# Optimization experiments

Measured on AMD Instinct MI355X. Metric: run time of the kernel, lower is better.

Reference implementation:

```python
import jax, jax.numpy as jnp
import numpy as np

N = 6144      # num_sample / nodes per graph
E = 196608    # edges per graph (avg degree 32)
F = 256       # input feature dim (same for all 4 graphs)
H = 256       # hidden_channels (== F so all SAGEConv layers are HxH)
D = 512       # fusion dim (hardcoded in module)
G = 4         # number of graphs
ATT = 128     # attention bottleneck (hardcoded)
WS = 0.05     # weight init scale


def setup_inputs() -> dict:
    key = jax.random.key(0)
    k = jax.random.split(key, 16)
    return {
        "xs": jax.random.normal(k[0], (G, N, F), jnp.float32),
        "edge_index": jax.random.randint(k[1], (G, 2, E), 0, N),
        "x_content": jax.random.normal(k[2], (N, F), jnp.float32),
        # SAGEConv params: per graph, 3 layers, lin_l (with bias) on aggregated
        # neighbors, lin_r (no bias) on root. F == H so all layers stack.
        "sage_Wl": jax.random.normal(k[3], (G, 3, H, H), jnp.float32) * WS,
        "sage_bl": jnp.zeros((G, 3, H), jnp.float32),
        "sage_Wr": jax.random.normal(k[4], (G, 3, H, H), jnp.float32) * WS,
        # lin1..lin4 : F -> 512
        "lin_W": jax.random.normal(k[5], (G, D, F), jnp.float32) * WS,
        "lin_b": jnp.zeros((G, D), jnp.float32),
        # ResidualFusion attention MLP 512 -> 128 -> 1, softmax over graph axis
        "att_W1": jax.random.normal(k[6], (ATT, D), jnp.float32) * WS,
        "att_b1": jnp.zeros((ATT,), jnp.float32),
        "att_W2": jax.random.normal(k[7], (1, ATT), jnp.float32) * WS,
        "att_b2": jnp.zeros((1,), jnp.float32),
        "res_W": jax.random.normal(k[8], (D, D), jnp.float32) * WS,
        "res_b": jnp.zeros((D,), jnp.float32),
        "fusion_weight": jnp.array([0.7, 0.3], jnp.float32),
        # SelfExpression coefficients, init 1e-8 * ones as in the module
        "C_content": jnp.full((N, N), 1e-8, jnp.float32),
        "C_structure": jnp.full((N, N), 1e-8, jnp.float32),
    }


def _gnn(x, ei, Wl, bl, Wr):
    # One GraphSAGE stack: 3 SAGEConv(mean) layers, relu after each,
    # dropout is identity in eval mode.
    src, dst = ei[0], ei[1]
    deg = jax.ops.segment_sum(jnp.ones((E,), x.dtype), dst, num_segments=N)
    deg = jnp.maximum(deg, 1.0)[:, None]
    for i in range(3):
        m = jax.ops.segment_sum(x[src], dst, num_segments=N) / deg  # mean aggr
        x = jax.nn.relu(m @ Wl[i].T + bl[i] + x @ Wr[i].T)
    return x


def reference(xs, edge_index, x_content, sage_Wl, sage_bl, sage_Wr,
              lin_W, lin_b, att_W1, att_b1, att_W2, att_b2,
              res_W, res_b, fusion_weight, C_content, C_structure):
    # Four GraphSAGE stacks, vmapped over the graph axis.
    xg = jax.vmap(_gnn)(xs, edge_index, sage_Wl, sage_bl, sage_Wr)  # [G,N,F]
    # lin1..lin4 -> [G,N,D]
    feats = jnp.einsum('gnf,gdf->gnd', xg, lin_W) + lin_b[:, None, :]
    # ResidualFusion: attention over stacked features, softmax over graph axis
    h = jax.nn.relu(jnp.einsum('gnd,kd->gnk', feats, att_W1) + att_b1)
    logits = jnp.einsum('gnk,ok->gno', h, att_W2) + att_b2  # [G,N,1]
    w = jax.nn.softmax(logits, axis=0)
    weighted = jnp.sum(w * feats, axis=0)            # [N,D]
    residual = feats[0] @ res_W.T + res_b            # [N,D]
    structure_features = jax.nn.relu(weighted + residual)
    # Coefficient fusion with softmax-normalized scalar weights
    fw = jax.nn.softmax(fusion_weight)
    fusion_expression = fw[0] * C_content + fw[1] * C_structure  # [N,N]
    return (fusion_expression, x_content, structure_features, C_content, C_structure)
```

## Files before the change

### kernel.cpp

```cpp
#include <hip/hip_runtime.h>
#include <hip/hip_bf16.h>

constexpr int N_ = 6144;
constexpr int E_ = 196608;
constexpr int F_ = 256;
constexpr int D_ = 512;
constexpr int G_ = 4;
constexpr int A_ = 128;

typedef short bf16x8 __attribute__((ext_vector_type(8)));
typedef float f32x4 __attribute__((ext_vector_type(4)));
typedef float f4 __attribute__((ext_vector_type(4)));
typedef int i4 __attribute__((ext_vector_type(4)));
typedef __hip_bfloat16 hb;

__device__ inline float b2f(unsigned short u) {
    union { unsigned u32; float f; } x; x.u32 = ((unsigned)u) << 16; return x.f;
}
__device__ inline unsigned short f2bu(float f) {
    hb b = __float2bfloat16(f);
    return *reinterpret_cast<unsigned short*>(&b);
}

#define GLD_LDS16(gp, lp) \
    __builtin_amdgcn_global_load_lds((const __attribute__((address_space(1))) void*)(gp), \
                                     (__attribute__((address_space(3))) void*)(lp), 16, 0, 0)

struct SP {
    const f4* Cc; const f4* Cs; const float* fw;
    f4* o0; f4* o3; f4* o4;
    long ib; long ie; int nsb;
};

__device__ void stream_slice(const SP sp, int sb)
{
    float fa = sp.fw[0], fb = sp.fw[1];
    float mx = fmaxf(fa, fb);
    float ea = expf(fa - mx), eb = expf(fb - mx);
    float w0 = ea / (ea + eb), w1 = eb / (ea + eb);
    const long S = (long)sp.nsb * blockDim.x;
    long i = sp.ib + (long)sb * blockDim.x + threadIdx.x;
    for (; i + 3 * S < sp.ie; i += 4 * S) {
        f4 a0 = __builtin_nontemporal_load(sp.Cc + i);
        f4 b0 = __builtin_nontemporal_load(sp.Cs + i);
        f4 a1 = __builtin_nontemporal_load(sp.Cc + i + S);
        f4 b1 = __builtin_nontemporal_load(sp.Cs + i + S);
        f4 a2 = __builtin_nontemporal_load(sp.Cc + i + 2 * S);
        f4 b2 = __builtin_nontemporal_load(sp.Cs + i + 2 * S);
        f4 a3 = __builtin_nontemporal_load(sp.Cc + i + 3 * S);
        f4 b3 = __builtin_nontemporal_load(sp.Cs + i + 3 * S);
        __builtin_nontemporal_store(a0, sp.o3 + i);
        __builtin_nontemporal_store(b0, sp.o4 + i);
        __builtin_nontemporal_store(w0 * a0 + w1 * b0, sp.o0 + i);
        __builtin_nontemporal_store(a1, sp.o3 + i + S);
        __builtin_nontemporal_store(b1, sp.o4 + i + S);
        __builtin_nontemporal_store(w0 * a1 + w1 * b1, sp.o0 + i + S);
        __builtin_nontemporal_store(a2, sp.o3 + i + 2 * S);
        __builtin_nontemporal_store(b2, sp.o4 + i + 2 * S);
        __builtin_nontemporal_store(w0 * a2 + w1 * b2, sp.o0 + i + 2 * S);
        __builtin_nontemporal_store(a3, sp.o3 + i + 3 * S);
        __builtin_nontemporal_store(b3, sp.o4 + i + 3 * S);
        __builtin_nontemporal_store(w0 * a3 + w1 * b3, sp.o0 + i + 3 * S);
    }
    for (; i < sp.ie; i += S) {
        f4 a = __builtin_nontemporal_load(sp.Cc + i);
        f4 b = __builtin_nontemporal_load(sp.Cs + i);
        __builtin_nontemporal_store(a, sp.o3 + i);
        __builtin_nontemporal_store(b, sp.o4 + i);
        __builtin_nontemporal_store(w0 * a + w1 * b, sp.o0 + i);
    }
}

__global__ void k_tail(SP sp) { stream_slice(sp, blockIdx.x); }

__global__ void k_prep(const float* __restrict__ xc, f4* __restrict__ o1,
                       const float* __restrict__ xs, ushort4* __restrict__ xsb,
                       const float* __restrict__ Wl, ushort4* __restrict__ Wlb,
                       const float* __restrict__ Wr, ushort4* __restrict__ Wrb,
                       const float* __restrict__ lin, ushort4* __restrict__ linb,
                       const float* __restrict__ aw, ushort4* __restrict__ awb,
                       const float* __restrict__ rw, ushort4* __restrict__ rwb,
                       i4* __restrict__ cursz, int PB, SP sp)
{
    if ((int)blockIdx.x < sp.nsb) { stream_slice(sp, blockIdx.x); return; }
    const int cb = blockIdx.x - sp.nsb;
    const long nz = (long)G_ * N_ / 4;
    const long n0 = (long)N_ * F_ / 4;
    const long n1 = (long)G_ * N_ * F_ / 4;
    const long n2 = (long)G_ * 3 * F_ * F_ / 4;
    const long n4 = (long)G_ * D_ * F_ / 4;
    const long n5 = (long)A_ * D_ / 4;
    const long n6 = (long)D_ * D_ / 4;
    const long T = nz + n0 + n1 + 2 * n2 + n4 + n5 + n6;
    long stride = (long)PB * blockDim.x;
    for (long u = (long)cb * blockDim.x + threadIdx.x; u < T; u += stride) {
        long v = u;
        if (v < nz) { cursz[v] = i4{0, 0, 0, 0}; continue; }
        v -= nz;
        if (v < n0) {
            f4 x = __builtin_nontemporal_load((const f4*)xc + v);
            __builtin_nontemporal_store(x, o1 + v);
            continue;
        }
        v -= n0;
        const float* s; ushort4* d;
        if (v < n1) { s = xs; d = xsb; }
        else {
            v -= n1;
            if (v < n2) { s = Wl; d = Wlb; }
            else {
                v -= n2;
                if (v < n2) { s = Wr; d = Wrb; }
                else {
                    v -= n2;
                    if (v < n4) { s = lin; d = linb; }
                    else {
                        v -= n4;
                        if (v < n5) { s = aw; d = awb; }
                        else { v -= n5; s = rw; d = rwb; }
                    }
                }
            }
        }
        f4 x = *((const f4*)s + v);
        ushort4 o;
        o.x = f2bu(x[0]); o.y = f2bu(x[1]); o.z = f2bu(x[2]); o.w = f2bu(x[3]);
        d[v] = o;
    }
}

__global__ void k_count(const int* __restrict__ ei, int* __restrict__ cnt, SP sp)
{
    if ((int)blockIdx.x < sp.nsb) { stream_slice(sp, blockIdx.x); return; }
    long i = (long)(blockIdx.x - sp.nsb) * blockDim.x + threadIdx.x;
    int g = (int)(i / E_);
    int e = (int)(i % E_);
    int dst = ei[(long)g * 2 * E_ + E_ + e];
    atomicAdd(&cnt[g * N_ + dst], 1);
}

__global__ void k_scan(int* __restrict__ cnt_cursor, int* __restrict__ row_ptr,
                       float* __restrict__ deg, SP sp)
{
    if ((int)blockIdx.x < sp.nsb) { stream_slice(sp, blockIdx.x); return; }
    int g = blockIdx.x - sp.nsb;
    __shared__ int swsum[16];
    __shared__ int s_off;
    const int lane = threadIdx.x & 63;
    const int wid = threadIdx.x >> 6;
    if (threadIdx.x == 0) s_off = 0;
    __syncthreads();
    for (int base = 0; base < N_; base += 1024) {
        int idx = g * N_ + base + threadIdx.x;
        int v = cnt_cursor[idx];
        int incl = v;
        #pragma unroll
        for (int d = 1; d < 64; d <<= 1) {
            int t = __shfl_up(incl, d);
            if (lane >= d) incl += t;
        }
        if (lane == 63) swsum[wid] = incl;
        __syncthreads();
        if (wid == 0 && lane < 16) {
            int sv = swsum[lane];
            #pragma unroll
            for (int d = 1; d < 16; d <<= 1) {
                int t = __shfl_up(sv, d);
                if (lane >= d) sv += t;
            }
            swsum[lane] = sv;
        }
        __syncthreads();
        int bse = s_off;
        int woff = wid ? swsum[wid - 1] : 0;
        int rp = bse + woff + incl - v;
        row_ptr[g * (N_ + 1) + base + threadIdx.x] = rp;
        cnt_cursor[idx] = rp;
        deg[idx] = (float)(v > 1 ? v : 1);
        __syncthreads();
        if (threadIdx.x == 0) s_off = bse + swsum[15];
        __syncthreads();
    }
    if (threadIdx.x == 0) row_ptr[g * (N_ + 1) + N_] = s_off;
}

__global__ void k_fill(const int* __restrict__ ei, int* __restrict__ cursor,
                       int* __restrict__ csr_src, SP sp)
{
    if ((int)blockIdx.x < sp.nsb) { stream_slice(sp, blockIdx.x); return; }
    long i = (long)(blockIdx.x - sp.nsb) * blockDim.x + threadIdx.x;
    int g = (int)(i / E_);
    int e = (int)(i % E_);
    int src = ei[(long)g * 2 * E_ + e];
    int dst = ei[(long)g * 2 * E_ + E_ + e];
    int pos = atomicAdd(&cursor[g * N_ + dst], 1);
    csr_src[(long)g * E_ + pos] = src;
}

__global__ __launch_bounds__(256) void k_aggregate(
    const hb* __restrict__ x, const int* __restrict__ csr_src,
    const int* __restrict__ row_ptr, const float* __restrict__ deg,
    hb* __restrict__ m, SP sp)
{
    if ((int)blockIdx.x < sp.nsb) { stream_slice(sp, blockIdx.x); return; }
    int b = blockIdx.x - sp.nsb;
    int g = (b & 7) >> 1;
    int idx = ((b >> 3) << 1) | (b & 1);
    int node = idx * 4 + (threadIdx.x >> 6);
    int lane = threadIdx.x & 63;
    int qq = lane >> 4;
    int l16 = (lane & 15) * 16;
    const hb* xg = x + (long)g * N_ * F_;
    const int* rp = row_ptr + g * (N_ + 1);
    const int* cs = csr_src + (long)g * E_;
    int s = __builtin_amdgcn_readfirstlane(rp[node]);
    int e = __builtin_amdgcn_readfirstlane(rp[node + 1]);
    float a[16] = {};
    #pragma unroll 4
    for (int j = s; j < e; j += 4) {
        if (j + qq < e) {
            int src = cs[j + qq];
            const bf16x8* p = (const bf16x8*)(xg + (long)src * F_ + l16);
            bf16x8 v0 = p[0], v1 = p[1];
            #pragma unroll
            for (int q = 0; q < 8; ++q) a[q]     += b2f((unsigned short)v0[q]);
            #pragma unroll
            for (int q = 0; q < 8; ++q) a[q + 8] += b2f((unsigned short)v1[q]);
        }
    }
    #pragma unroll
    for (int q = 0; q < 16; ++q) {
        a[q] += __shfl_xor(a[q], 16);
        a[q] += __shfl_xor(a[q], 32);
    }
    if (qq == 0) {
        float inv = 1.0f / deg[g * N_ + node];
        bf16x8 lo, hi;
        #pragma unroll
        for (int q = 0; q < 8; ++q) { lo[q] = (short)f2bu(a[q] * inv); hi[q] = (short)f2bu(a[q + 8] * inv); }
        *(bf16x8*)(m + ((long)g * N_ + node) * F_ + l16) = lo;
        *(bf16x8*)(m + ((long)g * N_ + node) * F_ + l16 + 8) = hi;
    }
}

template <bool DUAL, bool RELU, bool LOGITS, bool FUSEOUT, bool PIN>
__global__ __launch_bounds__(256) void k_mfma_nt(
    const hb* __restrict__ A1, const hb* __restrict__ B1,
    const hb* __restrict__ A2, const hb* __restrict__ B2,
    const float* __restrict__ bias, hb* __restrict__ C,
    int ncols, int nrows, int ng, int Nc, int K,
    long a_batch, long b_batch, long bias_batch, long c_batch,
    const float* __restrict__ W2, const float* __restrict__ b2,
    float* __restrict__ logits,
    const float* __restrict__ lgAll, const hb* __restrict__ fAll,
    float* __restrict__ o2,
    SP sp)
{
    if ((int)blockIdx.x < sp.nsb) { stream_slice(sp, blockIdx.x); return; }
    int b = blockIdx.x - sp.nsb;
    int g, col, row;
    if (PIN) {
        g = (b & 7) >> 1;
        int idx = ((b >> 3) << 1) | (b & 1);
        col = idx % ncols; row = idx / ncols;
    } else {
        col = b % ncols;
        int r2 = b / ncols;
        row = r2 % nrows; g = r2 / nrows;
    }
    const int row0 = row * 128;
    const int col0 = col * 128;

    const hb* A1p = A1 + (long)g * a_batch;
    const hb* B1p = B1 + (long)g * b_batch;
    const hb* A2p = nullptr;
    const hb* B2p = nullptr;
    if (DUAL) { A2p = A2 + (long)g * a_batch; B2p = B2 + (long)g * b_batch; }
    const float* biasp = bias + (long)g * bias_batch;
    hb* Cp = C + (long)g * c_batch;

    __shared__ hb As[128 * 64];
    __shared__ hb Bs[128 * 64];
    __shared__ float sLog[2][128];
    __shared__ float sW[128][4];

    const int tid = threadIdx.x;
    const int lane = tid & 63;
    const int wid = tid >> 6;
    const int wr = wid >> 1;
    const int wc = wid & 1;

    if (FUSEOUT) {
        if (tid < 128) {
            int rr = row0 + tid;
            float l0 = lgAll[rr], l1 = lgAll[N_ + rr], l2 = lgAll[2 * N_ + rr], l3 = lgAll[3 * N_ + rr];
            float mx = fmaxf(fmaxf(l0, l1), fmaxf(l2, l3));
            float e0 = expf(l0 - mx), e1 = expf(l1 - mx), e2 = expf(l2 - mx), e3 = expf(l3 - mx);
            float inv = 1.f / (e0 + e1 + e2 + e3);
            sW[tid][0] = e0 * inv; sW[tid][1] = e1 * inv;
            sW[tid][2] = e2 * inv; sW[tid][3] = e3 * inv;
        }
    }

    const int srow = tid >> 3;
    const int sk8  = (tid & 7) * 8;

    f32x4 acc[4][4] = {};

    const int fr  = lane & 15;
    const int fkq = (lane >> 4) * 8;

    const int npass = DUAL ? 2 : 1;
    for (int pass = 0; pass < npass; ++pass) {
        const hb* A = (DUAL && pass) ? A2p : A1p;
        const hb* B = (DUAL && pass) ? B2p : B1p;
        for (int k0 = 0; k0 < K; k0 += 64) {
            __syncthreads();
            #pragma unroll
            for (int c = 0; c < 4; ++c) {
                int r = c * 32 + srow;
                GLD_LDS16(A + (long)(row0 + r) * K + k0 + sk8, As + r * 64 + sk8);
                GLD_LDS16(B + (long)(col0 + r) * K + k0 + sk8, Bs + r * 64 + sk8);
            }
            __syncthreads();

            bf16x8 af[4][2], bfr[4][2];
            #pragma unroll
            for (int m = 0; m < 4; ++m)
                #pragma unroll
                for (int kk = 0; kk < 2; ++kk)
                    af[m][kk] = *(const bf16x8*)(As + (wr * 64 + m * 16 + fr) * 64 + kk * 32 + fkq);
            #pragma unroll
            for (int n = 0; n < 4; ++n)
                #pragma unroll
                for (int kk = 0; kk < 2; ++kk)
                    bfr[n][kk] = *(const bf16x8*)(Bs + (wc * 64 + n * 16 + fr) * 64 + kk * 32 + fkq);

            #pragma unroll
            for (int m = 0; m < 4; ++m)
                #pragma unroll
                for (int n = 0; n < 4; ++n)
                    #pragma unroll
                    for (int kk = 0; kk < 2; ++kk)
                        acc[m][n] = __builtin_amdgcn_mfma_f32_16x16x32_bf16(
                            af[m][kk], bfr[n][kk], acc[m][n], 0, 0, 0);
        }
    }

    const int r4 = (lane >> 4) * 4;
    const int cc = lane & 15;

    if (LOGITS) {
        float w2v[4], bv[4];
        #pragma unroll
        for (int n = 0; n < 4; ++n) {
            int c2 = wc * 64 + n * 16 + cc;
            w2v[n] = W2[c2];
            bv[n]  = biasp[c2];
        }
        #pragma unroll
        for (int m = 0; m < 4; ++m) {
            #pragma unroll
            for (int j = 0; j < 4; ++j) {
                float p = 0.f;
                #pragma unroll
                for (int n = 0; n < 4; ++n) {
                    float h = fmaxf(acc[m][n][j] + bv[n], 0.f);
                    p += h * w2v[n];
                }
                p += __shfl_xor(p, 1); p += __shfl_xor(p, 2);
                p += __shfl_xor(p, 4); p += __shfl_xor(p, 8);
                if (cc == 0) sLog[wc][wr * 64 + m * 16 + r4 + j] = p;
            }
        }
        __syncthreads();
        if (tid < 128)
            logits[(long)g * N_ + row0 + tid] = sLog[0][tid] + sLog[1][tid] + b2[0];
    } else if (FUSEOUT) {
        const unsigned short* fu = (const unsigned short*)fAll;
        #pragma unroll
        for (int m = 0; m < 4; ++m) {
            #pragma unroll
            for (int n = 0; n < 4; ++n) {
                int c2 = col0 + wc * 64 + n * 16 + cc;
                float bv = biasp[c2];
                #pragma unroll
                for (int j = 0; j < 4; ++j) {
                    int rl = wr * 64 + m * 16 + r4 + j;
                    int rr = row0 + rl;
                    float s = acc[m][n][j] + bv;
                    #pragma unroll
                    for (int gg = 0; gg < 4; ++gg)
                        s += sW[rl][gg] * b2f(fu[((long)gg * N_ + rr) * D_ + c2]);
                    __builtin_nontemporal_store(fmaxf(s, 0.f), o2 + (long)rr * D_ + c2);
                }
            }
        }
    } else {
        #pragma unroll
        for (int m = 0; m < 4; ++m) {
            #pragma unroll
            for (int n = 0; n < 4; ++n) {
                int c2 = col0 + wc * 64 + n * 16 + cc;
                float bv = biasp[c2];
                #pragma unroll
                for (int j = 0; j < 4; ++j) {
                    int rr = row0 + wr * 64 + m * 16 + r4 + j;
                    float v = acc[m][n][j] + bv;
                    if (RELU) v = fmaxf(v, 0.f);
                    Cp[(long)rr * Nc + c2] = __float2bfloat16(v);
                }
            }
        }
    }
}

extern "C" void kernel_launch(void* const* d_in, const int* in_sizes, int n_in,
                              void* d_out, int out_size, void* d_ws, size_t ws_size,
                              hipStream_t stream)
{
    const float* xs        = (const float*)d_in[0];
    const int*   ei        = (const int*)  d_in[1];
    const float* x_content = (const float*)d_in[2];
    const float* sage_Wl   = (const float*)d_in[3];
    const float* sage_bl   = (const float*)d_in[4];
    const float* sage_Wr   = (const float*)d_in[5];
    const float* lin_W     = (const float*)d_in[6];
    const float* lin_b     = (const float*)d_in[7];
    const float* att_W1    = (const float*)d_in[8];
    const float* att_b1    = (const float*)d_in[9];
    const float* att_W2    = (const float*)d_in[10];
    const float* att_b2    = (const float*)d_in[11];
    const float* res_W     = (const float*)d_in[12];
    const float* res_b     = (const float*)d_in[13];
    const float* fusion_w  = (const float*)d_in[14];
    const float* Cc        = (const float*)d_in[15];
    const float* Cs        = (const float*)d_in[16];

    float* out0 = (float*)d_out;
    float* out1 = out0 + (size_t)N_ * N_;
    float* out2 = out1 + (size_t)N_ * F_;
    float* out3 = out2 + (size_t)N_ * D_;
    float* out4 = out3 + (size_t)N_ * N_;

    char* w = (char*)d_ws;
    auto alloc = [&](size_t bytes) {
        char* p = w;
        w += (bytes + 255) & ~(size_t)255;
        return p;
    };
    hb* xsb   = (hb*)alloc((size_t)G_ * N_ * F_ * 2);
    hb* xA    = (hb*)alloc((size_t)G_ * N_ * F_ * 2);
    hb* xB    = (hb*)alloc((size_t)G_ * N_ * F_ * 2);
    hb* mb    = (hb*)alloc((size_t)G_ * N_ * F_ * 2);
    hb* feats = (hb*)alloc((size_t)G_ * N_ * D_ * 2);
    hb* Wlb   = (hb*)alloc((size_t)G_ * 3 * F_ * F_ * 2);
    hb* Wrb   = (hb*)alloc((size_t)G_ * 3 * F_ * F_ * 2);
    hb* linWb = (hb*)alloc((size_t)G_ * D_ * F_ * 2);
    hb* attWb = (hb*)alloc((size_t)A_ * D_ * 2);
    hb* resWb = (hb*)alloc((size_t)D_ * D_ * 2);
    float* logit = (float*)alloc((size_t)G_ * N_ * 4);
    float* deg   = (float*)alloc((size_t)G_ * N_ * 4);
    int*   rowp  = (int*)  alloc((size_t)G_ * (N_ + 1) * 4);
    int*   curs  = (int*)  alloc((size_t)G_ * N_ * 4);
    int*   csrc  = (int*)  alloc((size_t)G_ * E_ * 4);

    const long U = (long)N_ * N_ / 4;
    const int cum[14] = {0, 85, 110, 130, 160, 255, 325, 420, 490, 585, 655, 745, 815, 950};
    long B[14];
    for (int i = 0; i < 14; ++i) B[i] = U * cum[i] / 1000;
    const int PREPB   = 512;
    const int SB_PREP = 512;
    const int SB_FLAT = 256;
    const int SB_GEMM = 256;
    const int TAILB   = 1024;
    auto mkSP = [&](int i, int nsb) {
        SP sp;
        sp.Cc = (const f4*)Cc; sp.Cs = (const f4*)Cs; sp.fw = fusion_w;
        sp.o0 = (f4*)out0; sp.o3 = (f4*)out3; sp.o4 = (f4*)out4;
        sp.ib = B[i]; sp.ie = (i == 13) ? U : B[i + 1]; sp.nsb = nsb;
        return sp;
    };
    SP tail = mkSP(13, TAILB);

    k_prep<<<SB_PREP + PREPB, 256, 0, stream>>>(
        x_content, (f4*)out1, xs, (ushort4*)xsb,
        sage_Wl, (ushort4*)Wlb, sage_Wr, (ushort4*)Wrb,
        lin_W, (ushort4*)linWb, att_W1, (ushort4*)attWb, res_W, (ushort4*)resWb,
        (i4*)curs, PREPB, mkSP(0, SB_PREP));

    k_count<<<SB_FLAT + G_ * E_ / 256, 256, 0, stream>>>(ei, curs, mkSP(1, SB_FLAT));
    k_scan<<<SB_FLAT + G_, 1024, 0, stream>>>(curs, rowp, deg, mkSP(2, SB_FLAT));
    k_fill<<<SB_FLAT + G_ * E_ / 256, 256, 0, stream>>>(ei, curs, csrc, mkSP(3, SB_FLAT));

    const hb* xin = xsb;
    hb* xout = xA;
    for (int layer = 0; layer < 3; ++layer) {
        k_aggregate<<<SB_FLAT + G_ * N_ / 4, 256, 0, stream>>>(
            xin, csrc, rowp, deg, mb, mkSP(4 + 2 * layer, SB_FLAT));
        k_mfma_nt<true, true, false, false, true>
            <<<SB_GEMM + (F_ / 128) * (N_ / 128) * G_, 256, 0, stream>>>(
            mb, Wlb + (size_t)layer * F_ * F_,
            xin, Wrb + (size_t)layer * F_ * F_,
            sage_bl + (size_t)layer * F_, xout,
            F_ / 128, N_ / 128, G_, F_, F_,
            (long)N_ * F_, (long)3 * F_ * F_, (long)3 * F_, (long)N_ * F_,
            nullptr, nullptr, nullptr, nullptr, nullptr, nullptr,
            mkSP(5 + 2 * layer, SB_GEMM));
        xin = xout;
        xout = (layer == 0) ? xB : xA;
    }
    const hb* xg = xA;

    k_mfma_nt<false, false, false, false, true>
        <<<SB_GEMM + (D_ / 128) * (N_ / 128) * G_, 256, 0, stream>>>(
        xg, linWb, nullptr, nullptr, lin_b, feats,
        D_ / 128, N_ / 128, G_, D_, F_,
        (long)N_ * F_, (long)D_ * F_, (long)D_, (long)N_ * D_,
        nullptr, nullptr, nullptr, nullptr, nullptr, nullptr,
        mkSP(10, SB_GEMM));

    k_mfma_nt<false, true, true, false, true>
        <<<SB_GEMM + (A_ / 128) * (N_ / 128) * G_, 256, 0, stream>>>(
        feats, attWb, nullptr, nullptr, att_b1, nullptr,
        A_ / 128, N_ / 128, G_, A_, D_,
        (long)N_ * D_, 0L, 0L, 0L,
        att_W2, att_b2, logit, nullptr, nullptr, nullptr,
        mkSP(11, SB_GEMM));

    k_mfma_nt<false, false, false, true, false>
        <<<SB_GEMM + (D_ / 128) * (N_ / 128) * 1, 256, 0, stream>>>(
        feats, resWb, nullptr, nullptr, res_b, nullptr,
        D_ / 128, N_ / 128, 1, D_, D_,
        0L, 0L, 0L, 0L,
        nullptr, nullptr, nullptr, logit, feats, out2,
        mkSP(12, SB_GEMM));

    k_tail<<<TAILB, 256, 0, stream>>>(tail);
}
```

Before: 422.9 us.

## Fold edge counting into prep, add 128x64 SAGE GEMM, rebalance stream slices

Merges the degree-count atomics into the prep kernel and zeroes the counters with a memset instead, removing one launch. Adds a dedicated SAGE layer GEMM with 128x64 tiles, which doubles the block count to improve occupancy on the small F=256 output. Unrolls the copy and convert loops by four. Re-tunes how the N×N streaming work is split across kernels and changes the prep block counts. This adds code size and more atomic contention within the single prep kernel.

```diff
diff --git a/kernel.cpp b/kernel.cpp
--- a/kernel.cpp
+++ b/kernel.cpp
@@ -11,7 +11,6 @@
 typedef short bf16x8 __attribute__((ext_vector_type(8)));
 typedef float f32x4 __attribute__((ext_vector_type(4)));
 typedef float f4 __attribute__((ext_vector_type(4)));
-typedef int i4 __attribute__((ext_vector_type(4)));
 typedef __hip_bfloat16 hb;
 
 __device__ inline float b2f(unsigned short u) {
@@ -20,6 +19,11 @@
 __device__ inline unsigned short f2bu(float f) {
     hb b = __float2bfloat16(f);
     return *reinterpret_cast<unsigned short*>(&b);
+}
+__device__ inline ushort4 cvt4(f4 x) {
+    ushort4 o;
+    o.x = f2bu(x[0]); o.y = f2bu(x[1]); o.z = f2bu(x[2]); o.w = f2bu(x[3]);
+    return o;
 }
 
 #define GLD_LDS16(gp, lp) \
@@ -80,33 +84,56 @@
                        const float* __restrict__ lin, ushort4* __restrict__ linb,
                        const float* __restrict__ aw, ushort4* __restrict__ awb,
                        const float* __restrict__ rw, ushort4* __restrict__ rwb,
-                       i4* __restrict__ cursz, int PB, SP sp)
+                       const int* __restrict__ ei, int* __restrict__ cnt,
+                       int PB, SP sp)
 {
     if ((int)blockIdx.x < sp.nsb) { stream_slice(sp, blockIdx.x); return; }
     const int cb = blockIdx.x - sp.nsb;
-    const long nz = (long)G_ * N_ / 4;
-    const long n0 = (long)N_ * F_ / 4;
-    const long n1 = (long)G_ * N_ * F_ / 4;
-    const long n2 = (long)G_ * 3 * F_ * F_ / 4;
-    const long n4 = (long)G_ * D_ * F_ / 4;
-    const long n5 = (long)A_ * D_ / 4;
-    const long n6 = (long)D_ * D_ / 4;
-    const long T = nz + n0 + n1 + 2 * n2 + n4 + n5 + n6;
-    long stride = (long)PB * blockDim.x;
-    for (long u = (long)cb * blockDim.x + threadIdx.x; u < T; u += stride) {
-        long v = u;
-        if (v < nz) { cursz[v] = i4{0, 0, 0, 0}; continue; }
-        v -= nz;
-        if (v < n0) {
-            f4 x = __builtin_nontemporal_load((const f4*)xc + v);
-            __builtin_nontemporal_store(x, o1 + v);
-            continue;
-        }
-        v -= n0;
-        const float* s; ushort4* d;
-        if (v < n1) { s = xs; d = xsb; }
-        else {
-            v -= n1;
+    const long S = (long)PB * 256;
+    const long t0 = (long)cb * 256 + threadIdx.x;
+
+    {
+        const long n = (long)N_ * F_ / 4;
+        const f4* src = (const f4*)xc;
+        long i = t0;
+        for (; i + 3 * S < n; i += 4 * S) {
+            f4 x0 = __builtin_nontemporal_load(src + i);
+            f4 x1 = __builtin_nontemporal_load(src + i + S);
+            f4 x2 = __builtin_nontemporal_load(src + i + 2 * S);
+            f4 x3 = __builtin_nontemporal_load(src + i + 3 * S);
+            __builtin_nontemporal_store(x0, o1 + i);
+            __builtin_nontemporal_store(x1, o1 + i + S);
+            __builtin_nontemporal_store(x2, o1 + i + 2 * S);
+            __builtin_nontemporal_store(x3, o1 + i + 3 * S);
+        }
+        for (; i < n; i += S)
+            __builtin_nontemporal_store(__builtin_nontemporal_load(src + i), o1 + i);
+    }
+    {
+        const long n = (long)G_ * N_ * F_ / 4;
+        const f4* src = (const f4*)xs;
+        long i = t0;
+        for (; i + 3 * S < n; i += 4 * S) {
+            f4 x0 = src[i];
+            f4 x1 = src[i + S];
+            f4 x2 = src[i + 2 * S];
+            f4 x3 = src[i + 3 * S];
+            xsb[i] = cvt4(x0);
+            xsb[i + S] = cvt4(x1);
+            xsb[i + 2 * S] = cvt4(x2);
+            xsb[i + 3 * S] = cvt4(x3);
+        }
+        for (; i < n; i += S) xsb[i] = cvt4(src[i]);
+    }
+    {
+        const long n2 = (long)G_ * 3 * F_ * F_ / 4;
+        const long n4 = (long)G_ * D_ * F_ / 4;
+        const long n5 = (long)A_ * D_ / 4;
+        const long n6 = (long)D_ * D_ / 4;
+        const long T = 2 * n2 + n4 + n5 + n6;
+        for (long u = t0; u < T; u += S) {
+            long v = u;
+            const float* s; ushort4* d;
             if (v < n2) { s = Wl; d = Wlb; }
             else {
                 v -= n2;
@@ -121,22 +148,17 @@
                     }
                 }
             }
-        }
-        f4 x = *((const f4*)s + v);
-        ushort4 o;
-        o.x = f2bu(x[0]); o.y = f2bu(x[1]); o.z = f2bu(x[2]); o.w = f2bu(x[3]);
-        d[v] = o;
-    }
-}
-
-__global__ void k_count(const int* __restrict__ ei, int* __restrict__ cnt, SP sp)
-{
-    if ((int)blockIdx.x < sp.nsb) { stream_slice(sp, blockIdx.x); return; }
-    long i = (long)(blockIdx.x - sp.nsb) * blockDim.x + threadIdx.x;
-    int g = (int)(i / E_);
-    int e = (int)(i % E_);
-    int dst = ei[(long)g * 2 * E_ + E_ + e];
-    atomicAdd(&cnt[g * N_ + dst], 1);
+            d[v] = cvt4(((const f4*)s)[v]);
+        }
+    }
+    {
+        for (long i = t0; i < (long)G_ * E_; i += S) {
+            int g = (int)(i / E_);
+            int e = (int)(i % E_);
+            int dst = ei[(long)g * 2 * E_ + E_ + e];
+            atomicAdd(&cnt[g * N_ + dst], 1);
+        }
+    }
 }
 
 __global__ void k_scan(int* __restrict__ cnt_cursor, int* __restrict__ row_ptr,
@@ -243,10 +265,101 @@
     }
 }
 
-template <bool DUAL, bool RELU, bool LOGITS, bool FUSEOUT, bool PIN>
+__global__ __launch_bounds__(256) void k_sage64(
+    const hb* __restrict__ A1, const hb* __restrict__ B1,
+    const hb* __restrict__ A2, const hb* __restrict__ B2,
+    const float* __restrict__ bias, hb* __restrict__ C, SP sp)
+{
+    if ((int)blockIdx.x < sp.nsb) { stream_slice(sp, blockIdx.x); return; }
+    int b = blockIdx.x - sp.nsb;
+    int g = (b & 7) >> 1;
+    int idx = ((b >> 3) << 1) | (b & 1);
+    int col = idx & 3, row = idx >> 2;
+    const int row0 = row * 128, col0 = col * 64;
+
+    const hb* A1p = A1 + (long)g * N_ * F_;
+    const hb* A2p = A2 + (long)g * N_ * F_;
+    const hb* B1p = B1 + (long)g * 3 * F_ * F_;
+    const hb* B2p = B2 + (long)g * 3 * F_ * F_;
+    const float* biasp = bias + (long)g * 3 * F_;
+    hb* Cp = C + (long)g * N_ * F_;
+
+    __shared__ hb As[128 * 64];
+    __shared__ hb Bs[64 * 64];
+
+    const int tid = threadIdx.x;
+    const int lane = tid & 63;
+    const int wid = tid >> 6;
+    const int wr = wid >> 1, wc = wid & 1;
+    const int srow = tid >> 3;
+    const int sk8 = (tid & 7) * 8;
+    const int fr = lane & 15;
+    const int fkq = (lane >> 4) * 8;
+
+    f32x4 acc[4][2] = {};
+
+    #pragma unroll
+    for (int pass = 0; pass < 2; ++pass) {
+        const hb* A = pass ? A2p : A1p;
+        const hb* B = pass ? B2p : B1p;
+        for (int k0 = 0; k0 < F_; k0 += 64) {
+            __syncthreads();
+            #pragma unroll
+            for (int c = 0; c < 4; ++c) {
+                int r = c * 32 + srow;
+                GLD_LDS16(A + (long)(row0 + r) * F_ + k0 + sk8, As + r * 64 + sk8);
+            }
+            #pragma unroll
+            for (int c = 0; c < 2; ++c) {
+                int r = c * 32 + srow;
+                GLD_LDS16(B + (long)(col0 + r) * F_ + k0 + sk8, Bs + r * 64 + sk8);
+            }
+            __syncthreads();
+
+            bf16x8 af[4][2], bq[2][2];
+            #pragma unroll
+            for (int m = 0; m < 4; ++m)
+                #pragma unroll
+                for (int kk = 0; kk < 2; ++kk)
+                    af[m][kk] = *(const bf16x8*)(As + (wr * 64 + m * 16 + fr) * 64 + kk * 32 + fkq);
+            #pragma unroll
+            for (int n = 0; n < 2; ++n)
+                #pragma unroll
+                for (int kk = 0; kk < 2; ++kk)
+                    bq[n][kk] = *(const bf16x8*)(Bs + (wc * 32 + n * 16 + fr) * 64 + kk * 32 + fkq);
+
+            #pragma unroll
+            for (int m = 0; m < 4; ++m)
+                #pragma unroll
+                for (int n = 0; n < 2; ++n)
+                    #pragma unroll
+                    for (int kk = 0; kk < 2; ++kk)
+                        acc[m][n] = __builtin_amdgcn_mfma_f32_16x16x32_bf16(
+                            af[m][kk], bq[n][kk], acc[m][n], 0, 0, 0);
+        }
+    }
+
+    const int r4 = (lane >> 4) * 4;
+    const int cc = lane & 15;
+    #pragma unroll
+    for (int m = 0; m < 4; ++m) {
+        #pragma unroll
+        for (int n = 0; n < 2; ++n) {
+            int c2 = col0 + wc * 32 + n * 16 + cc;
+            float bv = biasp[c2];
+            #pragma unroll
+            for (int j = 0; j < 4; ++j) {
+                int rr = row0 + wr * 64 + m * 16 + r4 + j;
+                float v = fmaxf(acc[m][n][j] + bv, 0.f);
+                Cp[(long)rr * F_ + c2] = __float2bfloat16(v);
+            }
+        }
+    }
+}
+
+template <bool RELU, bool LOGITS, bool FUSEOUT, bool PIN>
 __global__ __launch_bounds__(256) void k_mfma_nt(
     const hb* __restrict__ A1, const hb* __restrict__ B1,
-    const hb* __restrict__ A2, const hb* __restrict__ B2,
     const float* __restrict__ bias, hb* __restrict__ C,
     int ncols, int nrows, int ng, int Nc, int K,
     long a_batch, long b_batch, long bias_batch, long c_batch,
@@ -273,9 +386,6 @@
 
     const hb* A1p = A1 + (long)g * a_batch;
     const hb* B1p = B1 + (long)g * b_batch;
-    const hb* A2p = nullptr;
-    const hb* B2p = nullptr;
-    if (DUAL) { A2p = A2 + (long)g * a_batch; B2p = B2 + (long)g * b_batch; }
     const float* biasp = bias + (long)g * bias_batch;
     hb* Cp = C + (long)g * c_batch;
 
@@ -310,41 +420,36 @@
     const int fr  = lane & 15;
     const int fkq = (lane >> 4) * 8;
 
-    const int npass = DUAL ? 2 : 1;
-    for (int pass = 0; pass < npass; ++pass) {
-        const hb* A = (DUAL && pass) ? A2p : A1p;
-        const hb* B = (DUAL && pass) ? B2p : B1p;
-        for (int k0 = 0; k0 < K; k0 += 64) {
-            __syncthreads();
-            #pragma unroll
-            for (int c = 0; c < 4; ++c) {
-                int r = c * 32 + srow;
-                GLD_LDS16(A + (long)(row0 + r) * K + k0 + sk8, As + r * 64 + sk8);
-                GLD_LDS16(B + (long)(col0 + r) * K + k0 + sk8, Bs + r * 64 + sk8);
-            }
-            __syncthreads();
-
-            bf16x8 af[4][2], bfr[4][2];
-            #pragma unroll
-            for (int m = 0; m < 4; ++m)
-                #pragma unroll
-                for (int kk = 0; kk < 2; ++kk)
-                    af[m][kk] = *(const bf16x8*)(As + (wr * 64 + m * 16 + fr) * 64 + kk * 32 + fkq);
+    for (int k0 = 0; k0 < K; k0 += 64) {
+        __syncthreads();
+        #pragma unroll
+        for (int c = 0; c < 4; ++c) {
+            int r = c * 32 + srow;
+            GLD_LDS16(A1p + (long)(row0 + r) * K + k0 + sk8, As + r * 64 + sk8);
+            GLD_LDS16(B1p + (long)(col0 + r) * K + k0 + sk8, Bs + r * 64 + sk8);
+        }
+        __syncthreads();
+
+        bf16x8 af[4][2], bfr[4][2];
+        #pragma unroll
+        for (int m = 0; m < 4; ++m)
+            #pragma unroll
+            for (int kk = 0; kk < 2; ++kk)
+                af[m][kk] = *(const bf16x8*)(As + (wr * 64 + m * 16 + fr) * 64 + kk * 32 + fkq);
+        #pragma unroll
+        for (int n = 0; n < 4; ++n)
+            #pragma unroll
+            for (int kk = 0; kk < 2; ++kk)
+                bfr[n][kk] = *(const bf16x8*)(Bs + (wc * 64 + n * 16 + fr) * 64 + kk * 32 + fkq);
+
+        #pragma unroll
+        for (int m = 0; m < 4; ++m)
             #pragma unroll
             for (int n = 0; n < 4; ++n)
                 #pragma unroll
                 for (int kk = 0; kk < 2; ++kk)
-                    bfr[n][kk] = *(const bf16x8*)(Bs + (wc * 64 + n * 16 + fr) * 64 + kk * 32 + fkq);
-
-            #pragma unroll
-            for (int m = 0; m < 4; ++m)
-                #pragma unroll
-                for (int n = 0; n < 4; ++n)
-                    #pragma unroll
-                    for (int kk = 0; kk < 2; ++kk)
-                        acc[m][n] = __builtin_amdgcn_mfma_f32_16x16x32_bf16(
-                            af[m][kk], bfr[n][kk], acc[m][n], 0, 0, 0);
-        }
+                    acc[m][n] = __builtin_amdgcn_mfma_f32_16x16x32_bf16(
+                        af[m][kk], bfr[n][kk], acc[m][n], 0, 0, 0);
     }
 
     const int r4 = (lane >> 4) * 4;
@@ -466,11 +571,11 @@
     int*   csrc  = (int*)  alloc((size_t)G_ * E_ * 4);
 
     const long U = (long)N_ * N_ / 4;
-    const int cum[14] = {0, 85, 110, 130, 160, 255, 325, 420, 490, 585, 655, 745, 815, 950};
+    const int cum[14] = {0, 100, 120, 150, 235, 300, 385, 450, 535, 600, 680, 760, 950, 1000};
     long B[14];
     for (int i = 0; i < 14; ++i) B[i] = U * cum[i] / 1000;
-    const int PREPB   = 512;
-    const int SB_PREP = 512;
+    const int PREPB   = 768;
+    const int SB_PREP = 448;
     const int SB_FLAT = 256;
     const int SB_GEMM = 256;
     const int TAILB   = 1024;
@@ -478,63 +583,63 @@
         SP sp;
         sp.Cc = (const f4*)Cc; sp.Cs = (const f4*)Cs; sp.fw = fusion_w;
         sp.o0 = (f4*)out0; sp.o3 = (f4*)out3; sp.o4 = (f4*)out4;
-        sp.ib = B[i]; sp.ie = (i == 13) ? U : B[i + 1]; sp.nsb = nsb;
+        sp.ib = B[i]; sp.ie = B[i + 1]; sp.nsb = nsb;
         return sp;
     };
-    SP tail = mkSP(13, TAILB);
+    SP tail;
+    tail.Cc = (const f4*)Cc; tail.Cs = (const f4*)Cs; tail.fw = fusion_w;
+    tail.o0 = (f4*)out0; tail.o3 = (f4*)out3; tail.o4 = (f4*)out4;
+    tail.ib = B[12]; tail.ie = U; tail.nsb = TAILB;
+
+    hipMemsetAsync(curs, 0, (size_t)G_ * N_ * 4, stream);
 
     k_prep<<<SB_PREP + PREPB, 256, 0, stream>>>(
         x_content, (f4*)out1, xs, (ushort4*)xsb,
         sage_Wl, (ushort4*)Wlb, sage_Wr, (ushort4*)Wrb,
         lin_W, (ushort4*)linWb, att_W1, (ushort4*)attWb, res_W, (ushort4*)resWb,
-        (i4*)curs, PREPB, mkSP(0, SB_PREP));
-
-    k_count<<<SB_FLAT + G_ * E_ / 256, 256, 0, stream>>>(ei, curs, mkSP(1, SB_FLAT));
-    k_scan<<<SB_FLAT + G_, 1024, 0, stream>>>(curs, rowp, deg, mkSP(2, SB_FLAT));
-    k_fill<<<SB_FLAT + G_ * E_ / 256, 256, 0, stream>>>(ei, curs, csrc, mkSP(3, SB_FLAT));
+        ei, curs, PREPB, mkSP(0, SB_PREP));
+
+    k_scan<<<SB_FLAT + G_, 1024, 0, stream>>>(curs, rowp, deg, mkSP(1, SB_FLAT));
+    k_fill<<<SB_FLAT + G_ * E_ / 256, 256, 0, stream>>>(ei, curs, csrc, mkSP(2, SB_FLAT));
 
     const hb* xin = xsb;
     hb* xout = xA;
     for (int layer = 0; layer < 3; ++layer) {
         k_aggregate<<<SB_FLAT + G_ * N_ / 4, 256, 0, stream>>>(
-            xin, csrc, rowp, deg, mb, mkSP(4 + 2 * layer, SB_FLAT));
-        k_mfma_nt<true, true, false, false, true>
-            <<<SB_GEMM + (F_ / 128) * (N_ / 128) * G_, 256, 0, stream>>>(
+            xin, csrc, rowp, deg, mb, mkSP(3 + 2 * layer, SB_FLAT));
+        k_sage64<<<SB_GEMM + 4 * (N_ / 128) * G_, 256, 0, stream>>>(
             mb, Wlb + (size_t)layer * F_ * F_,
             xin, Wrb + (size_t)layer * F_ * F_,
             sage_bl + (size_t)layer * F_, xout,
-            F_ / 128, N_ / 128, G_, F_, F_,
-            (long)N_ * F_, (long)3 * F_ * F_, (long)3 * F_, (long)N_ * F_,
-            nullptr, nullptr, nullptr, nullptr, nullptr, nullptr,
-            mkSP(5 + 2 * layer, SB_GEMM));
+            mkSP(4 + 2 * layer, SB_GEMM));
         xin = xout;
         xout = (layer == 0) ? xB : xA;
     }
     const hb* xg = xA;
 
-    k_mfma_nt<false, false, false, false, true>
+    k_mfma_nt<false, false, false, true>
         <<<SB_GEMM + (D_ / 128) * (N_ / 128) * G_, 256, 0, stream>>>(
-        xg, linWb, nullptr, nullptr, lin_b, feats,
+        xg, linWb, lin_b, feats,
         D_ / 128, N_ / 128, G_, D_, F_,
         (long)N_ * F_, (long)D_ * F_, (long)D_, (long)N_ * D_,
         nullptr, nullptr, nullptr, nullptr, nullptr, nullptr,
-        mkSP(10, SB_GEMM));
-
-    k_mfma_nt<false, true, true, false, true>
+        mkSP(9, SB_GEMM));
+
+    k_mfma_nt<true, true, false, true>
         <<<SB_GEMM + (A_ / 128) * (N_ / 128) * G_, 256, 0, stream>>>(
-        feats, attWb, nullptr, nullptr, att_b1, nullptr,
+        feats, attWb, att_b1, nullptr,
         A_ / 128, N_ / 128, G_, A_, D_,
         (long)N_ * D_, 0L, 0L, 0L,
         att_W2, att_b2, logit, nullptr, nullptr, nullptr,
-        mkSP(11, SB_GEMM));
-
-    k_mfma_nt<false, false, false, true, false>
+        mkSP(10, SB_GEMM));
+
+    k_mfma_nt<false, false, true, false>
         <<<SB_GEMM + (D_ / 128) * (N_ / 128) * 1, 256, 0, stream>>>(
-        feats, resWb, nullptr, nullptr, res_b, nullptr,
+        feats, resWb, res_b, nullptr,
         D_ / 128, N_ / 128, 1, D_, D_,
         0L, 0L, 0L, 0L,
         nullptr, nullptr, nullptr, logit, feats, out2,
-        mkSP(12, SB_GEMM));
+        mkSP(11, SB_GEMM));
 
     k_tail<<<TAILB, 256, 0, stream>>>(tail);
 }
```

Measured after the change: 405.7 us, median of 3. -4.1%, faster.
